# Kernel optimization log

Hardware: AMD Instinct MI355X
Metric: run time of the kernel (lower is better)

## Reference

```python
import jax, jax.numpy as jnp
import numpy as np

DECAY = 0.99
EPS = 1e-05


def setup_inputs() -> dict:
    key = jax.random.key(0)
    k1, k2 = jax.random.split(key)
    x = jax.random.normal(k1, (32, 2048, 128), dtype=jnp.float32)
    embed = jax.random.normal(k2, (1024, 128), dtype=jnp.float32)
    cluster_size = jnp.zeros((1024,), dtype=jnp.float32)
    embed_avg = embed  # register_buffer('embed_avg', embed.clone())
    return {"x": x, "embed": embed, "cluster_size": cluster_size, "embed_avg": embed_avg}


def reference(x, embed, cluster_size, embed_avg):
    N, D = embed.shape
    flat_x = x.reshape(-1, D)  # [T, D]
    distances = (
        jnp.sum(flat_x * flat_x, axis=1, keepdims=True)
        + jnp.sum(embed * embed, axis=1)
        - 2.0 * flat_x @ embed.T
    )  # [T, N]
    idx = jnp.argmin(distances, axis=1)  # [T]
    quantized = embed[idx].reshape(x.shape)
    # EMA codebook update (training branch); segment_sum replaces the one-hot matmuls
    counts = jax.ops.segment_sum(jnp.ones(flat_x.shape[0], dtype=x.dtype), idx, num_segments=N)
    embed_sums = jax.ops.segment_sum(flat_x, idx, num_segments=N)  # [N, D]
    new_cluster_size = DECAY * cluster_size + (1.0 - DECAY) * counts
    new_embed_avg = DECAY * embed_avg + (1.0 - DECAY) * embed_sums
    n = jnp.sum(new_cluster_size)
    cs = (new_cluster_size + EPS) / (n + N * EPS) * n
    new_embed = new_embed_avg / cs[:, None]
    # straight-through estimator
    out = x + jax.lax.stop_gradient(quantized - x)
    return out, new_embed, new_cluster_size, new_embed_avg
```

## Files before the change

kernel.cpp:

```cpp
#include <hip/hip_runtime.h>

#define NTOK   65536
#define NCODES 1024
#define DIM    128
#define BT     128
#define MARGIN 6.0f
#define CAP    2047

typedef __attribute__((ext_vector_type(8))) short short8;
typedef __attribute__((ext_vector_type(4))) float f32x4;

__device__ __forceinline__ unsigned short f2bf(float f) {
  unsigned u = __float_as_uint(f);
  u += 0x7FFFu + ((u >> 16) & 1u);
  return (unsigned short)(u >> 16);
}

__global__ __launch_bounds__(256) void prep_kernel(const float* __restrict__ E,
                                                   float* __restrict__ ee,
                                                   unsigned short* __restrict__ ebf) {
  #pragma clang fp contract(off)
  const int b = blockIdx.x;
  if (b < 64) {
    const int id = b * 256 + threadIdx.x;
    const int l  = id & 63;
    const int s  = (id >> 6) & 3;
    const int ct = id >> 8;
    const int c  = ct * 16 + (l & 15);
    const int ko = s * 32 + (l >> 4) * 8;
    const float4* p = (const float4*)(E + (size_t)c * DIM + ko);
    float4 A = p[0], B = p[1];
    short8 v;
    v[0]=f2bf(A.x); v[1]=f2bf(A.y); v[2]=f2bf(A.z); v[3]=f2bf(A.w);
    v[4]=f2bf(B.x); v[5]=f2bf(B.y); v[6]=f2bf(B.z); v[7]=f2bf(B.w);
    ((short8*)ebf)[id] = v;
  } else {
    const int c = (b - 64) * 256 + threadIdx.x;
    const float4* r4 = (const float4*)(E + (size_t)c * DIM);
    float v[DIM];
    #pragma unroll
    for (int i = 0; i < 32; ++i) {
      float4 q = r4[i];
      v[4*i] = q.x; v[4*i+1] = q.y; v[4*i+2] = q.z; v[4*i+3] = q.w;
    }
    float r[8];
    #pragma unroll
    for (int j = 0; j < 8; ++j) r[j] = v[j] * v[j];
    #pragma unroll
    for (int i = 1; i < 16; ++i) {
      #pragma unroll
      for (int j = 0; j < 8; ++j) { float s = v[8*i+j] * v[8*i+j]; r[j] = r[j] + s; }
    }
    ee[c] = ((r[0]+r[1])+(r[2]+r[3])) + ((r[4]+r[5])+(r[6]+r[7]));
  }
}

__global__ __launch_bounds__(256, 2) void vq_main(
    const float* __restrict__ X, const float* __restrict__ E,
    const unsigned short* __restrict__ ebf, const float* __restrict__ ee,
    float* __restrict__ out, int* __restrict__ idxg, int* __restrict__ cnt_i) {
  #pragma clang fp contract(off)
  __shared__ __align__(16) char x_lds[32768];
  __shared__ float bestA[4][BT];
  __shared__ float thrf[BT];
  __shared__ unsigned long long best64[BT];
  __shared__ int cand_n;
  __shared__ unsigned cand[CAP];

  const int tid  = threadIdx.x;
  const int lane = tid & 63;
  const int wv   = tid >> 6;
  const long blk = blockIdx.x;
  const float* Xb = X + (size_t)blk * BT * DIM;

  {
    const int r = tid >> 1, h = tid & 1;
    const float4* p4 = (const float4*)(Xb + r * DIM + h * 64);
    #pragma unroll
    for (int q = 0; q < 8; ++q) {
      float4 A = p4[2*q], B = p4[2*q+1];
      short8 v;
      v[0]=f2bf(A.x); v[1]=f2bf(A.y); v[2]=f2bf(A.z); v[3]=f2bf(A.w);
      v[4]=f2bf(B.x); v[5]=f2bf(B.y); v[6]=f2bf(B.z); v[7]=f2bf(B.w);
      const int o    = h * 8 + q;
      const int unit = (r >> 4) * 4 + (o >> 2);
      const int ln   = ((o & 3) << 4) | (r & 15);
      *(short8*)(x_lds + unit * 1024 + ln * 16) = v;
    }
  }

  short8 bfr[8][4];
  float  eev[8];
  const short8* ebv = (const short8*)ebf;

#define LOAD_SET(SET)                                                         \
  { _Pragma("unroll")                                                         \
    for (int ct = 0; ct < 8; ++ct) {                                          \
      _Pragma("unroll")                                                       \
      for (int s = 0; s < 4; ++s)                                             \
        bfr[ct][s] = ebv[(((SET) * 32 + wv * 8 + ct) * 4 + s) * 64 + lane];   \
      eev[ct] = ee[(SET) * 512 + wv * 128 + ct * 16 + (lane & 15)];           \
    } }

#define MFMA4(ACC, A0, A1, A2, A3, CT)                                        \
  ACC = __builtin_amdgcn_mfma_f32_16x16x32_bf16(A0, bfr[CT][0], ACC, 0, 0, 0);\
  ACC = __builtin_amdgcn_mfma_f32_16x16x32_bf16(A1, bfr[CT][1], ACC, 0, 0, 0);\
  ACC = __builtin_amdgcn_mfma_f32_16x16x32_bf16(A2, bfr[CT][2], ACC, 0, 0, 0);\
  ACC = __builtin_amdgcn_mfma_f32_16x16x32_bf16(A3, bfr[CT][3], ACC, 0, 0, 0);

#define SWEEP_MIN(FIRST)                                                      \
  for (int tt = 0; tt < 8; ++tt) {                                            \
    const char* xb = x_lds + tt * 4096 + lane * 16;                           \
    short8 a0 = *(const short8*)(xb);                                         \
    short8 a1 = *(const short8*)(xb + 1024);                                  \
    short8 a2 = *(const short8*)(xb + 2048);                                  \
    short8 a3 = *(const short8*)(xb + 3072);                                  \
    float bv0 = __builtin_inff(), bv1 = __builtin_inff();                     \
    float bv2 = __builtin_inff(), bv3 = __builtin_inff();                     \
    _Pragma("unroll")                                                         \
    for (int ct = 0; ct < 8; ++ct) {                                          \
      f32x4 acc = {0.f, 0.f, 0.f, 0.f};                                       \
      MFMA4(acc, a0, a1, a2, a3, ct)                                          \
      float d0 = eev[ct] - 2.0f * acc[0]; if (d0 < bv0) bv0 = d0;             \
      float d1 = eev[ct] - 2.0f * acc[1]; if (d1 < bv1) bv1 = d1;             \
      float d2 = eev[ct] - 2.0f * acc[2]; if (d2 < bv2) bv2 = d2;             \
      float d3 = eev[ct] - 2.0f * acc[3]; if (d3 < bv3) bv3 = d3;             \
    }                                                                         \
    _Pragma("unroll")                                                         \
    for (int m = 1; m < 16; m <<= 1) {                                        \
      float p0 = __shfl_xor(bv0, m, 64); if (p0 < bv0) bv0 = p0;              \
      float p1 = __shfl_xor(bv1, m, 64); if (p1 < bv1) bv1 = p1;              \
      float p2 = __shfl_xor(bv2, m, 64); if (p2 < bv2) bv2 = p2;              \
      float p3 = __shfl_xor(bv3, m, 64); if (p3 < bv3) bv3 = p3;              \
    }                                                                         \
    if ((lane & 15) == 0) {                                                   \
      const int tok = tt * 16 + (lane >> 4) * 4;                              \
      if (FIRST) {                                                            \
        bestA[wv][tok]     = bv0; bestA[wv][tok + 1] = bv1;                   \
        bestA[wv][tok + 2] = bv2; bestA[wv][tok + 3] = bv3;                   \
      } else {                                                                \
        if (bv0 < bestA[wv][tok])     bestA[wv][tok]     = bv0;               \
        if (bv1 < bestA[wv][tok + 1]) bestA[wv][tok + 1] = bv1;               \
        if (bv2 < bestA[wv][tok + 2]) bestA[wv][tok + 2] = bv2;               \
        if (bv3 < bestA[wv][tok + 3]) bestA[wv][tok + 3] = bv3;               \
      }                                                                       \
    }                                                                         \
  }

#define EMIT(D, RG, TH, CODE, TT)                                             \
  if ((D) < (TH)) {                                                           \
    int sl = atomicAdd(&cand_n, 1);                                           \
    if (sl < CAP)                                                             \
      cand[sl] = ((unsigned)((TT) * 16 + (lane >> 4) * 4 + (RG)) << 10)       \
               | (unsigned)(CODE);                                            \
  }

#define SWEEP_EMIT(CB)                                                        \
  for (int tt = 0; tt < 8; ++tt) {                                            \
    const char* xb = x_lds + tt * 4096 + lane * 16;                           \
    short8 a0 = *(const short8*)(xb);                                         \
    short8 a1 = *(const short8*)(xb + 1024);                                  \
    short8 a2 = *(const short8*)(xb + 2048);                                  \
    short8 a3 = *(const short8*)(xb + 3072);                                  \
    const float4 th4 = *(const float4*)(thrf + tt * 16 + (lane >> 4) * 4);    \
    _Pragma("unroll")                                                         \
    for (int ct = 0; ct < 8; ++ct) {                                          \
      f32x4 acc = {0.f, 0.f, 0.f, 0.f};                                       \
      MFMA4(acc, a0, a1, a2, a3, ct)                                          \
      const int code = (CB) + ct * 16 + (lane & 15);                          \
      float d0 = eev[ct] - 2.0f * acc[0]; EMIT(d0, 0, th4.x, code, tt)        \
      float d1 = eev[ct] - 2.0f * acc[1]; EMIT(d1, 1, th4.y, code, tt)        \
      float d2 = eev[ct] - 2.0f * acc[2]; EMIT(d2, 2, th4.z, code, tt)        \
      float d3 = eev[ct] - 2.0f * acc[3]; EMIT(d3, 3, th4.w, code, tt)        \
    }                                                                         \
  }

  LOAD_SET(0)
  __syncthreads();

  SWEEP_MIN(1)
  LOAD_SET(1)
  SWEEP_MIN(0)
  __syncthreads();

  if (tid < BT) {
    float m0 = bestA[0][tid], m1 = bestA[1][tid];
    float m2 = bestA[2][tid], m3 = bestA[3][tid];
    float mm = fminf(fminf(m0, m1), fminf(m2, m3));
    thrf[tid]   = mm + MARGIN;
    best64[tid] = ~0ull;
  }
  if (tid == 0) cand_n = 0;
  __syncthreads();

  SWEEP_EMIT(512 + wv * 128)
  LOAD_SET(0)
  SWEEP_EMIT(wv * 128)
  __syncthreads();

  {
    int cn = cand_n;
    const int nc = cn < CAP ? cn : CAP;
    for (int i = tid; i < nc; i += 256) {
      const unsigned pc = cand[i];
      const int t = pc >> 10, c = pc & 1023;
      const float* xr = Xb + t * DIM;
      const float* er = E + (size_t)c * DIM;
      float dot = 0.0f;
      #pragma unroll
      for (int k = 0; k < DIM; ++k) dot = __builtin_fmaf(xr[k], er[k], dot);
      float d = ee[c] - 2.0f * dot;
      unsigned u = __float_as_uint(d);
      u ^= (unsigned)((int)u >> 31) | 0x80000000u;
      unsigned long long key = ((unsigned long long)u << 32) | (unsigned)c;
      atomicMin(best64 + t, key);
    }
  }
  __syncthreads();

  if (tid < BT) {
    const int c0 = (int)(best64[tid] & 1023ull);
    idxg[blk * BT + tid] = c0;
    atomicAdd(cnt_i + c0, 1);
  }
  const int tt2 = tid >> 1, hf = tid & 1;
  const int fi2 = (int)(best64[tt2] & 1023ull);
  const float* xrow = Xb  + tt2 * DIM + hf * 64;
  const float* erow = E   + ((size_t)fi2 << 7) + hf * 64;
  float*       orow = out + ((size_t)blk * BT + tt2) * DIM + hf * 64;
  #pragma unroll
  for (int q = 0; q < 16; ++q) {
    float4 xv = *(const float4*)(xrow + q * 4);
    float4 ev = *(const float4*)(erow + q * 4);
    float4 o;
    o.x = xv.x + (ev.x - xv.x);
    o.y = xv.y + (ev.y - xv.y);
    o.z = xv.z + (ev.z - xv.z);
    o.w = xv.w + (ev.w - xv.w);
    *(float4*)(orow + q * 4) = o;
  }
}

__global__ __launch_bounds__(1024) void prefix_fin1(
    const float* __restrict__ cluster_size, const int* __restrict__ cnt_i,
    float* __restrict__ out_cs, float* __restrict__ cs_ws,
    int* __restrict__ cursor, int* __restrict__ offs) {
  #pragma clang fp contract(off)
  __shared__ float red[1024];
  __shared__ int   sc[1024];
  const int n = threadIdx.x;
  const int cnt = cnt_i[n];
  float ncs = 0.99f * cluster_size[n] + 0.01f * (float)cnt;
  out_cs[n] = ncs;
  red[n] = ncs;
  sc[n]  = cnt;
  __syncthreads();
  for (int s = 512; s > 0; s >>= 1) {
    if (n < s) red[n] = red[n] + red[n + s];
    __syncthreads();
  }
  float ntot = red[0];
  cs_ws[n] = (ncs + 1e-5f) / (ntot + 0.01024f) * ntot;
  for (int d = 1; d < 1024; d <<= 1) {
    int t = (n >= d) ? sc[n - d] : 0;
    __syncthreads();
    sc[n] += t;
    __syncthreads();
  }
  int excl = sc[n] - cnt;
  cursor[n] = excl;
  offs[n]   = excl;
}

__global__ __launch_bounds__(256) void scatter_kernel(
    const int* __restrict__ idxg, int* __restrict__ cursor,
    int* __restrict__ order) {
  const int t  = blockIdx.x * 256 + threadIdx.x;
  const int fi = idxg[t];
  const int slot = atomicAdd(cursor + fi, 1);
  order[slot] = t;
}

__global__ __launch_bounds__(256) void sums_chunk(
    const float* __restrict__ X, const int* __restrict__ order,
    const int* __restrict__ idxg, float* __restrict__ sums) {
  #pragma clang fp contract(off)
  const int lane = threadIdx.x & 63;
  const int base = blockIdx.x * 256 + (threadIdx.x >> 6) * 64;
  const int tl = order[base + lane];
  const int cl = idxg[tl];
  float ax = 0.f, ay = 0.f;
  int cprev = __shfl(cl, 0, 64);
  #pragma unroll
  for (int j0 = 0; j0 < 64; j0 += 8) {
    int tj[8], cj[8];
    float2 buf[8];
    #pragma unroll
    for (int q = 0; q < 8; ++q) tj[q] = __shfl(tl, j0 + q, 64);
    #pragma unroll
    for (int q = 0; q < 8; ++q)
      buf[q] = *((const float2*)(X + ((size_t)tj[q] << 7)) + lane);
    #pragma unroll
    for (int q = 0; q < 8; ++q) cj[q] = __shfl(cl, j0 + q, 64);
    #pragma unroll
    for (int q = 0; q < 8; ++q) {
      if (cj[q] != cprev) {
        atomicAdd(sums + cprev * DIM + lane * 2,     ax);
        atomicAdd(sums + cprev * DIM + lane * 2 + 1, ay);
        ax = 0.f; ay = 0.f; cprev = cj[q];
      }
      ax = ax + buf[q].x;
      ay = ay + buf[q].y;
    }
  }
  atomicAdd(sums + cprev * DIM + lane * 2,     ax);
  atomicAdd(sums + cprev * DIM + lane * 2 + 1, ay);
}

__global__ __launch_bounds__(256) void finalize2(
    const float* __restrict__ embed_avg, const float* __restrict__ sums,
    const float* __restrict__ cs_ws, float* __restrict__ out_embed,
    float* __restrict__ out_avg) {
  #pragma clang fp contract(off)
  int i = blockIdx.x * 256 + threadIdx.x;
  float av = 0.99f * embed_avg[i] + 0.01f * sums[i];
  out_avg[i]   = av;
  out_embed[i] = av / cs_ws[i >> 7];
}

extern "C" void kernel_launch(void* const* d_in, const int* in_sizes, int n_in,
                              void* d_out, int out_size, void* d_ws, size_t ws_size,
                              hipStream_t stream) {
  const float* X  = (const float*)d_in[0];
  const float* E  = (const float*)d_in[1];
  const float* CS = (const float*)d_in[2];
  const float* EA = (const float*)d_in[3];
  float* out = (float*)d_out;
  float* ws  = (float*)d_ws;

  int*   cnt_i  = (int*)ws;
  float* sums   = ws + 1024;
  float* eearr  = ws + 132096;
  float* csarr  = ws + 133120;
  int*   cursor = (int*)(ws + 134144);
  int*   offs   = (int*)(ws + 135168);
  int*   idxarr = (int*)(ws + 136192);
  int*   order  = (int*)(ws + 201728);
  unsigned short* ebf = (unsigned short*)(ws + 267264);

  hipMemsetAsync(d_ws, 0, 132096 * sizeof(float), stream);

  prep_kernel   <<<68,           256, 0, stream>>>(E, eearr, ebf);
  vq_main       <<<NTOK / BT,    256, 0, stream>>>(X, E, ebf, eearr, out,
                                                   idxarr, cnt_i);
  prefix_fin1   <<<1, 1024, 0, stream>>>(CS, cnt_i, out + 8519680, csarr,
                                         cursor, offs);
  scatter_kernel<<<NTOK / 256,   256, 0, stream>>>(idxarr, cursor, order);
  sums_chunk    <<<NTOK / 256,   256, 0, stream>>>(X, order, idxarr, sums);
  finalize2     <<<131072 / 256, 256, 0, stream>>>(EA, sums, csarr,
                                                   out + 8388608, out + 8520704);
}
```

Baseline: 165.0 us.

## Halve codebook register tiles to raise VQ kernel occupancy; fold memset into prep

The main VQ kernel now keeps 4 codebook tiles in registers instead of 8 and sweeps the codebook in four sets rather than two. The launch bound rises to 4 blocks per CU. LDS use is also cut: the candidate cap shrinks and best64 now aliases the bestA buffer after an added barrier. The workspace memset is replaced by extra zeroing blocks inside the prep kernel, which removes one launch. In exchange there are more LDS reloads of the X fragments per sweep, and a smaller candidate buffer that could overflow.

Measured after the change: 181.8 us. +10.2%, slower.

```diff
diff --git a/kernel.cpp b/kernel.cpp
--- a/kernel.cpp
+++ b/kernel.cpp
@@ -5,7 +5,7 @@
 #define DIM    128
 #define BT     128
 #define MARGIN 6.0f
-#define CAP    2047
+#define CAP    1200
 
 typedef __attribute__((ext_vector_type(8))) short short8;
 typedef __attribute__((ext_vector_type(4))) float f32x4;
@@ -18,7 +18,8 @@
 
 __global__ __launch_bounds__(256) void prep_kernel(const float* __restrict__ E,
                                                    float* __restrict__ ee,
-                                                   unsigned short* __restrict__ ebf) {
+                                                   unsigned short* __restrict__ ebf,
+                                                   float* __restrict__ zero_base) {
   #pragma clang fp contract(off)
   const int b = blockIdx.x;
   if (b < 64) {
@@ -34,7 +35,7 @@
     v[0]=f2bf(A.x); v[1]=f2bf(A.y); v[2]=f2bf(A.z); v[3]=f2bf(A.w);
     v[4]=f2bf(B.x); v[5]=f2bf(B.y); v[6]=f2bf(B.z); v[7]=f2bf(B.w);
     ((short8*)ebf)[id] = v;
-  } else {
+  } else if (b < 68) {
     const int c = (b - 64) * 256 + threadIdx.x;
     const float4* r4 = (const float4*)(E + (size_t)c * DIM);
     float v[DIM];
@@ -52,18 +53,20 @@
       for (int j = 0; j < 8; ++j) { float s = v[8*i+j] * v[8*i+j]; r[j] = r[j] + s; }
     }
     ee[c] = ((r[0]+r[1])+(r[2]+r[3])) + ((r[4]+r[5])+(r[6]+r[7]));
-  }
-}
-
-__global__ __launch_bounds__(256, 2) void vq_main(
+  } else {
+    float4 z = {0.f, 0.f, 0.f, 0.f};
+    ((float4*)zero_base)[(b - 68) * 256 + threadIdx.x] = z;
+  }
+}
+
+__global__ __launch_bounds__(256, 4) void vq_main(
     const float* __restrict__ X, const float* __restrict__ E,
     const unsigned short* __restrict__ ebf, const float* __restrict__ ee,
     float* __restrict__ out, int* __restrict__ idxg, int* __restrict__ cnt_i) {
   #pragma clang fp contract(off)
   __shared__ __align__(16) char x_lds[32768];
-  __shared__ float bestA[4][BT];
-  __shared__ float thrf[BT];
-  __shared__ unsigned long long best64[BT];
+  __shared__ __align__(16) float bestA[4][BT];
+  __shared__ __align__(16) float thrf[BT];
   __shared__ int cand_n;
   __shared__ unsigned cand[CAP];
 
@@ -89,17 +92,18 @@
     }
   }
 
-  short8 bfr[8][4];
-  float  eev[8];
+  short8 bfr[4][4];
+  float  eev[4];
   const short8* ebv = (const short8*)ebf;
 
 #define LOAD_SET(SET)                                                         \
   { _Pragma("unroll")                                                         \
-    for (int ct = 0; ct < 8; ++ct) {                                          \
+    for (int ct = 0; ct < 4; ++ct) {                                          \
+      const int tile = wv * 16 + (SET) * 4 + ct;                              \
       _Pragma("unroll")                                                       \
       for (int s = 0; s < 4; ++s)                                             \
-        bfr[ct][s] = ebv[(((SET) * 32 + wv * 8 + ct) * 4 + s) * 64 + lane];   \
-      eev[ct] = ee[(SET) * 512 + wv * 128 + ct * 16 + (lane & 15)];           \
+        bfr[ct][s] = ebv[(tile * 4 + s) * 64 + lane];                         \
+      eev[ct] = ee[tile * 16 + (lane & 15)];                                  \
     } }
 
 #define MFMA4(ACC, A0, A1, A2, A3, CT)                                        \
@@ -118,7 +122,7 @@
     float bv0 = __builtin_inff(), bv1 = __builtin_inff();                     \
     float bv2 = __builtin_inff(), bv3 = __builtin_inff();                     \
     _Pragma("unroll")                                                         \
-    for (int ct = 0; ct < 8; ++ct) {                                          \
+    for (int ct = 0; ct < 4; ++ct) {                                          \
       f32x4 acc = {0.f, 0.f, 0.f, 0.f};                                       \
       MFMA4(acc, a0, a1, a2, a3, ct)                                          \
       float d0 = eev[ct] - 2.0f * acc[0]; if (d0 < bv0) bv0 = d0;             \
@@ -155,7 +159,7 @@
                | (unsigned)(CODE);                                            \
   }
 
-#define SWEEP_EMIT(CB)                                                        \
+#define SWEEP_EMIT(SET)                                                       \
   for (int tt = 0; tt < 8; ++tt) {                                            \
     const char* xb = x_lds + tt * 4096 + lane * 16;                           \
     short8 a0 = *(const short8*)(xb);                                         \
@@ -164,10 +168,10 @@
     short8 a3 = *(const short8*)(xb + 3072);                                  \
     const float4 th4 = *(const float4*)(thrf + tt * 16 + (lane >> 4) * 4);    \
     _Pragma("unroll")                                                         \
-    for (int ct = 0; ct < 8; ++ct) {                                          \
+    for (int ct = 0; ct < 4; ++ct) {                                          \
       f32x4 acc = {0.f, 0.f, 0.f, 0.f};                                       \
       MFMA4(acc, a0, a1, a2, a3, ct)                                          \
-      const int code = (CB) + ct * 16 + (lane & 15);                          \
+      const int code = (wv * 16 + (SET) * 4 + ct) * 16 + (lane & 15);         \
       float d0 = eev[ct] - 2.0f * acc[0]; EMIT(d0, 0, th4.x, code, tt)        \
       float d1 = eev[ct] - 2.0f * acc[1]; EMIT(d1, 1, th4.y, code, tt)        \
       float d2 = eev[ct] - 2.0f * acc[2]; EMIT(d2, 2, th4.z, code, tt)        \
@@ -181,21 +185,30 @@
   SWEEP_MIN(1)
   LOAD_SET(1)
   SWEEP_MIN(0)
+  LOAD_SET(2)
+  SWEEP_MIN(0)
+  LOAD_SET(3)
+  SWEEP_MIN(0)
   __syncthreads();
 
   if (tid < BT) {
     float m0 = bestA[0][tid], m1 = bestA[1][tid];
     float m2 = bestA[2][tid], m3 = bestA[3][tid];
-    float mm = fminf(fminf(m0, m1), fminf(m2, m3));
-    thrf[tid]   = mm + MARGIN;
-    best64[tid] = ~0ull;
-  }
+    thrf[tid] = fminf(fminf(m0, m1), fminf(m2, m3)) + MARGIN;
+  }
+  __syncthreads();
+  unsigned long long* best64 = (unsigned long long*)&bestA[0][0];
+  if (tid < BT) best64[tid] = ~0ull;
   if (tid == 0) cand_n = 0;
   __syncthreads();
 
-  SWEEP_EMIT(512 + wv * 128)
+  SWEEP_EMIT(3)
   LOAD_SET(0)
-  SWEEP_EMIT(wv * 128)
+  SWEEP_EMIT(0)
+  LOAD_SET(1)
+  SWEEP_EMIT(1)
+  LOAD_SET(2)
+  SWEEP_EMIT(2)
   __syncthreads();
 
   {
@@ -348,9 +361,7 @@
   int*   order  = (int*)(ws + 201728);
   unsigned short* ebf = (unsigned short*)(ws + 267264);
 
-  hipMemsetAsync(d_ws, 0, 132096 * sizeof(float), stream);
-
-  prep_kernel   <<<68,           256, 0, stream>>>(E, eearr, ebf);
+  prep_kernel   <<<197,          256, 0, stream>>>(E, eearr, ebf, ws);
   vq_main       <<<NTOK / BT,    256, 0, stream>>>(X, E, ebf, eearr, out,
                                                    idxarr, cnt_i);
   prefix_fin1   <<<1, 1024, 0, stream>>>(CS, cnt_i, out + 8519680, csarr,
```
